# Kernel tuning notes

Hardware: AMD Instinct MI355X
Metric: run time of the kernel (lower is better)

Reference implementation:

```python
import jax, jax.numpy as jnp
import numpy as np


def setup_inputs() -> dict:
    key = jax.random.key(0)
    k1, _ = jax.random.split(key)
    x = jax.random.normal(k1, (8, 128, 56, 56), dtype=jnp.float32)
    gamma = jnp.array(0.5, dtype=jnp.float32)  # learned scalar (init gamma=0.5)
    return {"x": x, "gamma": gamma}


def reference(x, gamma):
    # conv=False path: query/key/value convs are Identity, so Q=K=V=x flattened.
    B, C, H, W = x.shape
    N = H * W
    v = x.reshape(B, C, N)                          # [B, C, N]
    # energy[b, i, j] = sum_c x[b, c, i] * x[b, c, j]  (Q^T K)
    energy = jnp.einsum('bci,bcj->bij', v, v)       # [B, N, N]
    # multiplicative mask: zero out the diagonal BEFORE softmax (not -inf)
    mask = 1.0 - jnp.eye(N, dtype=energy.dtype)
    attention = jax.nn.softmax(energy * mask, axis=-1)  # [B, N, N]
    # out = bmm(V, attention): out[b, c, j] = sum_i v[b, c, i] * attention[b, i, j]
    out = jnp.einsum('bci,bij->bcj', v, attention)  # [B, C, N]
    out = jax.nn.relu(out).reshape(B, C, H, W)
    y = gamma * out + x
    return (y, out, x, gamma)
```

## Files before the change

### kernel.cpp

```cpp
#include <hip/hip_runtime.h>
#include <math.h>

#define Bb 8
#define Cc 128
#define Nn 3136
#define Np 3200
#define Mm (Bb*Cc*Nn)
#define PADX 136
#define PADV 72
#define SHIFT2 63.4785818f
#define SSCALE 1.2011224087f

#define EXP2F(v) __builtin_amdgcn_exp2f(v)

typedef unsigned short u16;
typedef unsigned int   u32;
typedef __attribute__((ext_vector_type(8)))  u16      u16x8;
typedef __attribute__((ext_vector_type(8)))  _Float16 f16x8;
typedef __attribute__((ext_vector_type(4)))  _Float16 f16x4;
typedef __attribute__((ext_vector_type(4)))  float    f32x4;
typedef __attribute__((ext_vector_type(16))) float    f32x16;

__global__ __launch_bounds__(256) void prep_kernel(const float* __restrict__ x,
                                                   const float* __restrict__ gamma_p,
                                                   float* __restrict__ out,
                                                   u16* __restrict__ xt,
                                                   u16* __restrict__ xc,
                                                   float* __restrict__ row_d) {
    const int bx = blockIdx.x;
    const int b = bx / 50, nblk = bx % 50;
    const int t = threadIdx.x;

    if (nblk == 49) {
        const u16x8 z8 = {0, 0, 0, 0, 0, 0, 0, 0};
        #pragma unroll
        for (int it = 0; it < 4; ++it) {
            const int idx = it * 256 + t, row = idx / 17, seg = idx % 17;
            *(u16x8*)&xt[(size_t)(b * Np + Nn + row) * PADX + seg * 8] = z8;
        }
        if (t < 64) {
            const int idx = 1024 + t, row = idx / 17, seg = idx % 17;
            *(u16x8*)&xt[(size_t)(b * Np + Nn + row) * PADX + seg * 8] = z8;
        }
        #pragma unroll
        for (int it = 0; it < 4; ++it) {
            const int idx = it * 256 + t, c = idx >> 3, seg = idx & 7;
            *(u16x8*)&xc[(size_t)(b * Cc + c) * Np + Nn + seg * 8] = z8;
        }
        if (t < 64) row_d[b * Np + Nn + t] = 1.0f;
        return;
    }

    __shared__ float lx[Cc][65];
    const int n0 = nblk * 64;

    #pragma unroll 8
    for (int r = 0; r < 32; ++r) {
        const int c = r * 4 + (t >> 6);
        const int g = (b * Cc + c) * Nn + n0 + (t & 63);
        const float v = x[g];
        lx[c][t & 63] = v;
        out[(size_t)2 * Mm + g] = v;
    }
    __syncthreads();

    {
        const int nl = t & 63, cseg = t >> 6;
        u16x8 hv[4];
        #pragma unroll
        for (int cc = 0; cc < 32; ++cc) {
            const _Float16 hh = (_Float16)(lx[cseg * 32 + cc][nl] * SSCALE);
            hv[cc >> 3][cc & 7] = __builtin_bit_cast(u16, hh);
        }
        const size_t base = (size_t)(b * Np + n0 + nl) * PADX + cseg * 32;
        #pragma unroll
        for (int k = 0; k < 4; ++k) *(u16x8*)&xt[base + k * 8] = hv[k];
    }
    {
        const int c = t >> 1, half = t & 1;
        u16x8 hv[4];
        #pragma unroll
        for (int k = 0; k < 32; ++k) {
            const _Float16 hh = (_Float16)lx[c][half * 32 + k];
            hv[k >> 3][k & 7] = __builtin_bit_cast(u16, hh);
        }
        const size_t base = (size_t)(b * Cc + c) * Np + n0 + half * 32;
        #pragma unroll
        for (int k = 0; k < 4; ++k) *(u16x8*)&xc[base + k * 8] = hv[k];
    }
    if (bx == 0 && t == 0) out[(size_t)3 * Mm] = gamma_p[0];
}

__global__ __launch_bounds__(256, 3) void stats_kernel(const u16* __restrict__ xt,
                                                       float* __restrict__ row_d) {
    __shared__ u16 s_jt[64 * PADX];

    const int bx = blockIdx.x;
    const int b = bx / 98, rem = bx % 98;
    const int i0 = (rem >> 1) * 64, jh = rem & 1;
    const int t = threadIdx.x;
    const int w = t >> 6, l = t & 63, lane = l & 31, h = l >> 5;
    const int igrp = w & 1, jsub = w >> 1;

    f16x8 Bf[8];
    {
        const size_t rb = (size_t)(b * Np + i0 + igrp * 32 + lane) * PADX + h * 8;
        #pragma unroll
        for (int kk = 0; kk < 8; ++kk)
            Bf[kk] = *(const f16x8*)&xt[rb + kk * 16];
    }

    float sa = 0.0f, sb = 0.0f;
    const int jt0 = jh * 25;

    for (int jt = jt0; jt < jt0 + 25; ++jt) {
        const int j0 = jt * 64;
        __syncthreads();
        {
            const u16* src = xt + (size_t)(b * Np + j0) * PADX;
            u16x8 tv[4], tv4;
            #pragma unroll
            for (int it = 0; it < 4; ++it)
                tv[it] = *(const u16x8*)&src[(it * 256 + t) * 8];
            if (t < 64) tv4 = *(const u16x8*)&src[(1024 + t) * 8];
            #pragma unroll
            for (int it = 0; it < 4; ++it)
                *(u16x8*)&s_jt[(it * 256 + t) * 8] = tv[it];
            if (t < 64) *(u16x8*)&s_jt[(1024 + t) * 8] = tv4;
        }
        __syncthreads();

        f32x16 ea, eb;
        #pragma unroll
        for (int r = 0; r < 16; ++r) { ea[r] = 0.0f; eb[r] = 0.0f; }
        const int arow = (jsub * 32 + lane) * PADX + h * 8;
        #pragma unroll
        for (int kk = 0; kk < 4; ++kk) {
            const f16x8 A0 = *(const f16x8*)&s_jt[arow + (2 * kk) * 16];
            const f16x8 A1 = *(const f16x8*)&s_jt[arow + (2 * kk + 1) * 16];
            ea = __builtin_amdgcn_mfma_f32_32x32x16_f16(A0, Bf[2 * kk], ea, 0, 0, 0);
            eb = __builtin_amdgcn_mfma_f32_32x32x16_f16(A1, Bf[2 * kk + 1], eb, 0, 0, 0);
        }

        const bool diag = (j0 == i0) && (jsub == igrp);
        #pragma unroll
        for (int r = 0; r < 16; ++r) {
            const int mrow = (r & 3) + 8 * (r >> 2) + 4 * h;
            float v = ea[r] + eb[r];
            if (diag && (mrow == lane)) v = 0.0f;
            if (r & 1) sb += EXP2F(v - SHIFT2); else sa += EXP2F(v - SHIFT2);
        }
    }

    float ssum = sa + sb;
    ssum += __shfl_xor(ssum, 32, 64);
    if (h == 0) atomicAdd(&row_d[b * Np + i0 + igrp * 32 + lane], ssum);
}

__global__ __launch_bounds__(256, 3) void out_kernel(const u16* __restrict__ xt,
                                                     const u16* __restrict__ xc,
                                                     const float* __restrict__ row_d,
                                                     float* __restrict__ out) {
    __shared__ u16 s_xt[64 * PADX];
    __shared__ u16 s_xc[Cc * PADV];
    __shared__ u16 s_pt[64 * PADV];

    const int bx = blockIdx.x;
    const int b = bx / 98, rem = bx % 98;
    const int j0 = (rem >> 1) * 64, half = rem & 1;
    const int t = threadIdx.x;
    const int w = t >> 6, l = t & 63, lane = l & 31, h = l >> 5;
    const int isub = w & 1, jgrp = w >> 1;
    const int jg = w & 1,  cp = w >> 1;
    const u16* __restrict__ xtb = xt + (size_t)b * Np * PADX;
    const u16* __restrict__ xcb = xc + (size_t)b * Cc * Np;

    f16x8 Bj[8];
    {
        const size_t rb = (size_t)(j0 + jgrp * 32 + lane) * PADX + h * 8;
        #pragma unroll
        for (int kk = 0; kk < 8; ++kk)
            Bj[kk] = *(const f16x8*)&xtb[rb + kk * 16];
    }

    f32x16 oa, ob;
    #pragma unroll
    for (int r = 0; r < 16; ++r) { oa[r] = 0.0f; ob[r] = 0.0f; }

    for (int ti = 0; ti < 25; ++ti) {
        const int i0g = (half * 25 + ti) * 64;
        __syncthreads();
        {
            const u16* srct = xtb + (size_t)i0g * PADX;
            u16x8 vt[4], vt4, vcr[4];
            #pragma unroll
            for (int it = 0; it < 4; ++it) {
                vt[it] = *(const u16x8*)&srct[(it * 256 + t) * 8];
                const int q = it * 256 + t;
                vcr[it] = *(const u16x8*)&xcb[(size_t)(q >> 3) * Np + i0g + (q & 7) * 8];
            }
            if (t < 64) vt4 = *(const u16x8*)&srct[(1024 + t) * 8];
            #pragma unroll
            for (int it = 0; it < 4; ++it) {
                *(u16x8*)&s_xt[(it * 256 + t) * 8] = vt[it];
                const int q = it * 256 + t;
                *(u16x8*)&s_xc[(q >> 3) * PADV + (q & 7) * 8] = vcr[it];
            }
            if (t < 64) *(u16x8*)&s_xt[(1024 + t) * 8] = vt4;
        }
        __syncthreads();

        f32x16 ea, eb;
        #pragma unroll
        for (int r = 0; r < 16; ++r) { ea[r] = 0.0f; eb[r] = 0.0f; }
        const int arow = (isub * 32 + lane) * PADX + h * 8;
        #pragma unroll
        for (int kk = 0; kk < 4; ++kk) {
            const f16x8 A0 = *(const f16x8*)&s_xt[arow + (2 * kk) * 16];
            const f16x8 A1 = *(const f16x8*)&s_xt[arow + (2 * kk + 1) * 16];
            ea = __builtin_amdgcn_mfma_f32_32x32x16_f16(A0, Bj[2 * kk], ea, 0, 0, 0);
            eb = __builtin_amdgcn_mfma_f32_32x32x16_f16(A1, Bj[2 * kk + 1], eb, 0, 0, 0);
        }

        const bool mayDiag = (j0 < i0g + 64) && (i0g < j0 + 64);
        const int ptbase = (jgrp * 32 + lane) * PADV + isub * 32;
        #pragma unroll
        for (int q = 0; q < 4; ++q) {
            const f32x4 dq = *(const f32x4*)&row_d[b * Np + i0g + isub * 32 + q * 8 + h * 4];
            f16x4 pv;
            #pragma unroll
            for (int r = 0; r < 4; ++r) {
                const int m = q * 8 + h * 4 + r;
                float v = ea[q * 4 + r] + eb[q * 4 + r];
                if (mayDiag && (i0g + isub * 32 + m == j0 + jgrp * 32 + lane)) v = 0.0f;
                pv[r] = (_Float16)(EXP2F(v - SHIFT2) * __builtin_amdgcn_rcpf(dq[r]));
            }
            *(f16x4*)&s_pt[ptbase + q * 8 + h * 4] = pv;
        }
        __syncthreads();

        const int pbrow = (jg * 32 + lane) * PADV + h * 8;
        const int va0 = (cp * 64 + lane) * PADV + h * 8;
        const int va1 = va0 + 32 * PADV;
        #pragma unroll
        for (int kk = 0; kk < 4; ++kk) {
            const f16x8 Bp  = *(const f16x8*)&s_pt[pbrow + kk * 16];
            const f16x8 Av0 = *(const f16x8*)&s_xc[va0 + kk * 16];
            const f16x8 Av1 = *(const f16x8*)&s_xc[va1 + kk * 16];
            oa = __builtin_amdgcn_mfma_f32_32x32x16_f16(Av0, Bp, oa, 0, 0, 0);
            ob = __builtin_amdgcn_mfma_f32_32x32x16_f16(Av1, Bp, ob, 0, 0, 0);
        }
    }

    float* __restrict__ slotp = out + (size_t)half * Mm;
    #pragma unroll
    for (int r = 0; r < 16; ++r) {
        const int mrow = (r & 3) + 8 * (r >> 2) + 4 * h;
        const int jj = j0 + jg * 32 + lane;
        slotp[(size_t)(b * Cc + cp * 64 + mrow) * Nn + jj] = oa[r];
        slotp[(size_t)(b * Cc + cp * 64 + 32 + mrow) * Nn + jj] = ob[r];
    }
}

__global__ __launch_bounds__(256) void reduce_kernel(const float* __restrict__ x,
                                                     const float* __restrict__ gamma_p,
                                                     float* __restrict__ out) {
    const float gamma = gamma_p[0];
    float* __restrict__ s0 = out;
    float* __restrict__ s1 = out + (size_t)Mm;
    const size_t base = (size_t)blockIdx.x * 4096 + threadIdx.x * 4;
    #pragma unroll
    for (int it = 0; it < 4; ++it) {
        const size_t k = base + it * 1024;
        const f32x4 p0 = *(const f32x4*)&s0[k];
        const f32x4 p1 = *(const f32x4*)&s1[k];
        const f32x4 xv = *(const f32x4*)&x[k];
        f32x4 o, y;
        #pragma unroll
        for (int r = 0; r < 4; ++r) {
            o[r] = fmaxf(p0[r] + p1[r], 0.0f);
            y[r] = fmaf(gamma, o[r], xv[r]);
        }
        *(f32x4*)&s0[k] = y;
        *(f32x4*)&s1[k] = o;
    }
}

extern "C" void kernel_launch(void* const* d_in, const int* in_sizes, int n_in,
                              void* d_out, int out_size, void* d_ws, size_t ws_size,
                              hipStream_t stream) {
    const float* x       = (const float*)d_in[0];
    const float* gamma_p = (const float*)d_in[1];
    float* out = (float*)d_out;

    float* row_d = (float*)d_ws;
    u16* xt = (u16*)((char*)d_ws + (1 << 17));
    u16* xc = xt + (size_t)Bb * Np * PADX;

    (void)hipMemsetAsync(row_d, 0, (size_t)Bb * Np * sizeof(float), stream);
    prep_kernel  <<<400, 256, 0, stream>>>(x, gamma_p, out, xt, xc, row_d);
    stats_kernel <<<784, 256, 0, stream>>>(xt, row_d);
    out_kernel   <<<784, 256, 0, stream>>>(xt, xc, row_d, out);
    reduce_kernel<<<784, 256, 0, stream>>>(x, gamma_p, out);
}
```

Measured before the change: 209.7 us.

## Use direct global-to-LDS loads and pre-tile xc into padded LDS layout

Replaces register-staged global-to-shared copies in the stats and out kernels with global_load_lds DMA, so tile data goes straight into LDS without passing through VGPRs. To let the xc tile be copied contiguously, prep_kernel now writes xc as per-tile blocks already in the padded PADV layout, and zero-fills the last tile. This cuts register pressure and load/store instructions in the main loops. The cost is more workspace for the padded layout and a reliance on the per-wave LDS base addressing of the builtin.

Measured after the change: 208.8 us. About the same (-0.4%).

```diff
diff --git a/kernel.cpp b/kernel.cpp
--- a/kernel.cpp
+++ b/kernel.cpp
@@ -21,11 +21,17 @@
 typedef __attribute__((ext_vector_type(4)))  float    f32x4;
 typedef __attribute__((ext_vector_type(16))) float    f32x16;
 
+__device__ __forceinline__ void dma16(const u16* g, u16* l) {
+    __builtin_amdgcn_global_load_lds(
+        (const __attribute__((address_space(1))) u32*)(const void*)g,
+        (__attribute__((address_space(3))) u32*)(void*)l, 16, 0, 0);
+}
+
 __global__ __launch_bounds__(256) void prep_kernel(const float* __restrict__ x,
                                                    const float* __restrict__ gamma_p,
                                                    float* __restrict__ out,
                                                    u16* __restrict__ xt,
-                                                   u16* __restrict__ xc,
+                                                   u16* __restrict__ xcp,
                                                    float* __restrict__ row_d) {
     const int bx = blockIdx.x;
     const int b = bx / 50, nblk = bx % 50;
@@ -42,11 +48,12 @@
             const int idx = 1024 + t, row = idx / 17, seg = idx % 17;
             *(u16x8*)&xt[(size_t)(b * Np + Nn + row) * PADX + seg * 8] = z8;
         }
-        #pragma unroll
-        for (int it = 0; it < 4; ++it) {
-            const int idx = it * 256 + t, c = idx >> 3, seg = idx & 7;
-            *(u16x8*)&xc[(size_t)(b * Cc + c) * Np + Nn + seg * 8] = z8;
-        }
+        u16* tile49 = xcp + (size_t)(b * 50 + 49) * Cc * PADV;
+        #pragma unroll
+        for (int it = 0; it < 4; ++it)
+            *(u16x8*)&tile49[(it * 256 + t) * 8] = z8;
+        if (t < 128)
+            *(u16x8*)&tile49[(1024 + t) * 8] = z8;
         if (t < 64) row_d[b * Np + Nn + t] = 1.0f;
         return;
     }
@@ -84,9 +91,9 @@
             const _Float16 hh = (_Float16)lx[c][half * 32 + k];
             hv[k >> 3][k & 7] = __builtin_bit_cast(u16, hh);
         }
-        const size_t base = (size_t)(b * Cc + c) * Np + n0 + half * 32;
-        #pragma unroll
-        for (int k = 0; k < 4; ++k) *(u16x8*)&xc[base + k * 8] = hv[k];
+        const size_t base = ((size_t)(b * 50 + nblk) * Cc + c) * PADV + half * 32;
+        #pragma unroll
+        for (int k = 0; k < 4; ++k) *(u16x8*)&xcp[base + k * 8] = hv[k];
     }
     if (bx == 0 && t == 0) out[(size_t)3 * Mm] = gamma_p[0];
 }
@@ -101,6 +108,7 @@
     const int t = threadIdx.x;
     const int w = t >> 6, l = t & 63, lane = l & 31, h = l >> 5;
     const int igrp = w & 1, jsub = w >> 1;
+    const int wb = t & ~63;
 
     f16x8 Bf[8];
     {
@@ -118,15 +126,10 @@
         __syncthreads();
         {
             const u16* src = xt + (size_t)(b * Np + j0) * PADX;
-            u16x8 tv[4], tv4;
             #pragma unroll
             for (int it = 0; it < 4; ++it)
-                tv[it] = *(const u16x8*)&src[(it * 256 + t) * 8];
-            if (t < 64) tv4 = *(const u16x8*)&src[(1024 + t) * 8];
-            #pragma unroll
-            for (int it = 0; it < 4; ++it)
-                *(u16x8*)&s_jt[(it * 256 + t) * 8] = tv[it];
-            if (t < 64) *(u16x8*)&s_jt[(1024 + t) * 8] = tv4;
+                dma16(&src[(it * 256 + t) * 8], &s_jt[(it * 256 + wb) * 8]);
+            if (t < 64) dma16(&src[(1024 + t) * 8], &s_jt[(1024 + wb) * 8]);
         }
         __syncthreads();
 
@@ -158,7 +161,7 @@
 }
 
 __global__ __launch_bounds__(256, 3) void out_kernel(const u16* __restrict__ xt,
-                                                     const u16* __restrict__ xc,
+                                                     const u16* __restrict__ xcp,
                                                      const float* __restrict__ row_d,
                                                      float* __restrict__ out) {
     __shared__ u16 s_xt[64 * PADX];
@@ -172,8 +175,8 @@
     const int w = t >> 6, l = t & 63, lane = l & 31, h = l >> 5;
     const int isub = w & 1, jgrp = w >> 1;
     const int jg = w & 1,  cp = w >> 1;
+    const int wb = t & ~63;
     const u16* __restrict__ xtb = xt + (size_t)b * Np * PADX;
-    const u16* __restrict__ xcb = xc + (size_t)b * Cc * Np;
 
     f16x8 Bj[8];
     {
@@ -188,25 +191,19 @@
     for (int r = 0; r < 16; ++r) { oa[r] = 0.0f; ob[r] = 0.0f; }
 
     for (int ti = 0; ti < 25; ++ti) {
-        const int i0g = (half * 25 + ti) * 64;
+        const int tile = half * 25 + ti;
+        const int i0g = tile * 64;
         __syncthreads();
         {
             const u16* srct = xtb + (size_t)i0g * PADX;
-            u16x8 vt[4], vt4, vcr[4];
+            const u16* srcc = xcp + (size_t)(b * 50 + tile) * Cc * PADV;
             #pragma unroll
             for (int it = 0; it < 4; ++it) {
-                vt[it] = *(const u16x8*)&srct[(it * 256 + t) * 8];
-                const int q = it * 256 + t;
-                vcr[it] = *(const u16x8*)&xcb[(size_t)(q >> 3) * Np + i0g + (q & 7) * 8];
+                dma16(&srct[(it * 256 + t) * 8], &s_xt[(it * 256 + wb) * 8]);
+                dma16(&srcc[(it * 256 + t) * 8], &s_xc[(it * 256 + wb) * 8]);
             }
-            if (t < 64) vt4 = *(const u16x8*)&srct[(1024 + t) * 8];
-            #pragma unroll
-            for (int it = 0; it < 4; ++it) {
-                *(u16x8*)&s_xt[(it * 256 + t) * 8] = vt[it];
-                const int q = it * 256 + t;
-                *(u16x8*)&s_xc[(q >> 3) * PADV + (q & 7) * 8] = vcr[it];
-            }
-            if (t < 64) *(u16x8*)&s_xt[(1024 + t) * 8] = vt4;
+            if (t < 64)  dma16(&srct[(1024 + t) * 8], &s_xt[(1024 + wb) * 8]);
+            if (t < 128) dma16(&srcc[(1024 + t) * 8], &s_xc[(1024 + wb) * 8]);
         }
         __syncthreads();
 
@@ -294,12 +291,12 @@
     float* out = (float*)d_out;
 
     float* row_d = (float*)d_ws;
-    u16* xt = (u16*)((char*)d_ws + (1 << 17));
-    u16* xc = xt + (size_t)Bb * Np * PADX;
+    u16* xt  = (u16*)((char*)d_ws + (1 << 17));
+    u16* xcp = xt + (size_t)Bb * Np * PADX;
 
     (void)hipMemsetAsync(row_d, 0, (size_t)Bb * Np * sizeof(float), stream);
-    prep_kernel  <<<400, 256, 0, stream>>>(x, gamma_p, out, xt, xc, row_d);
+    prep_kernel  <<<400, 256, 0, stream>>>(x, gamma_p, out, xt, xcp, row_d);
     stats_kernel <<<784, 256, 0, stream>>>(xt, row_d);
-    out_kernel   <<<784, 256, 0, stream>>>(xt, xc, row_d, out);
+    out_kernel   <<<784, 256, 0, stream>>>(xt, xcp, row_d, out);
     reduce_kernel<<<784, 256, 0, stream>>>(x, gamma_p, out);
 }
```
